# Kernel tuning notes

Hardware: AMD Instinct MI355X
Metric: run time of the kernel (lower is better)

The kernel has to match this reference:

```python
import jax, jax.numpy as jnp
import numpy as np

N_NODES = 100000


def _graph_conv(x, W, b, src, dst, deg_out, deg_in, relu):
    # DGL GraphConv, norm='both':
    #   h = (x * D_out^{-1/2}) W ; agg = scatter_sum over edges ; out = agg * D_in^{-1/2} + b
    norm_src = jax.lax.rsqrt(jnp.maximum(deg_out, 1.0))  # [N]
    norm_dst = jax.lax.rsqrt(jnp.maximum(deg_in, 1.0))   # [N]
    h = (x * norm_src[:, None]) @ W                       # [N, d_out]
    agg = jax.ops.segment_sum(h[src], dst, num_segments=N_NODES)  # [N, d_out]
    out = agg * norm_dst[:, None] + b
    return jax.nn.relu(out) if relu else out


def setup_inputs() -> dict:
    key = jax.random.key(0)
    ks = jax.random.split(key, 8)
    E = 1600000
    in_dim, hid_dim, out_dim = 128, 128, 64
    feat = jax.random.normal(ks[0], (N_NODES, in_dim), dtype=jnp.float32)
    edge_index = jax.random.randint(ks[1], (2, E), 0, N_NODES, dtype=jnp.int64)
    s = 1.0 / np.sqrt(in_dim)
    sh = 1.0 / np.sqrt(hid_dim)
    return {
        "feat": feat,
        "edge_index": edge_index,
        "W0": jax.random.normal(ks[2], (in_dim, hid_dim), dtype=jnp.float32) * s,
        "b0": jnp.zeros((hid_dim,), dtype=jnp.float32),
        "W1": jax.random.normal(ks[3], (hid_dim, hid_dim), dtype=jnp.float32) * sh,
        "b1": jnp.zeros((hid_dim,), dtype=jnp.float32),
        "W2": jax.random.normal(ks[4], (hid_dim, out_dim), dtype=jnp.float32) * sh,
        "b2": jnp.zeros((out_dim,), dtype=jnp.float32),
    }


def reference(feat, edge_index, W0, b0, W1, b1, W2, b2):
    src, dst = edge_index[0], edge_index[1]
    ones = jnp.ones(src.shape, dtype=feat.dtype)
    deg_out = jax.ops.segment_sum(ones, src, num_segments=N_NODES)  # src out-degree
    deg_in = jax.ops.segment_sum(ones, dst, num_segments=N_NODES)   # dst in-degree
    h = _graph_conv(feat, W0, b0, src, dst, deg_out, deg_in, relu=True)
    h = _graph_conv(h, W1, b1, src, dst, deg_out, deg_in, relu=True)
    h = _graph_conv(h, W2, b2, src, dst, deg_out, deg_in, relu=False)
    return h
```

## Files before the change

### kernel.cpp

```cpp
#include <hip/hip_runtime.h>
#include <hip/hip_fp16.h>


typedef _Float16 h8 __attribute__((ext_vector_type(8)));
typedef float f32x4 __attribute__((ext_vector_type(4)));

#define HWORDS 25024
#define NHS 32
#define NHD 256

__global__ __launch_bounds__(256) void k_pre(const int* __restrict__ src,
                                             const int* __restrict__ dst, int E,
                                             unsigned* __restrict__ histo_s,
                                             unsigned* __restrict__ histo_d,
                                             const float* __restrict__ W0,
                                             const float* __restrict__ W1,
                                             const float* __restrict__ W2,
                                             __half* __restrict__ Wt0,
                                             __half* __restrict__ Wt1,
                                             __half* __restrict__ Wt2) {
    __shared__ unsigned H[HWORDS];
    const int b = blockIdx.x;
    if (b < NHS + NHD) {
        const bool isS = b < NHS;
        const int c = isS ? b : b - NHS;
        const int NC = isS ? NHS : NHD;
        const int* arr = isS ? src : dst;
        unsigned* outp = (isS ? histo_s : histo_d) + (size_t)c * HWORDS;
        for (int i = threadIdx.x; i < HWORDS; i += 256) H[i] = 0;
        __syncthreads();
        const int perB = ((E + NC - 1) / NC + 3) & ~3;
        const int e0 = min(c * perB, E), e1 = min(e0 + perB, E);
        int i = e0 + threadIdx.x * 4;
        for (; i + 3 < e1; i += 1024) {
            int4 s4 = *(const int4*)(arr + i);
            atomicAdd(&H[s4.x >> 2], 1u << ((s4.x & 3) * 8));
            atomicAdd(&H[s4.y >> 2], 1u << ((s4.y & 3) * 8));
            atomicAdd(&H[s4.z >> 2], 1u << ((s4.z & 3) * 8));
            atomicAdd(&H[s4.w >> 2], 1u << ((s4.w & 3) * 8));
        }
        for (; i < e1; ++i) {
            int s = arr[i];
            atomicAdd(&H[s >> 2], 1u << ((s & 3) * 8));
        }
        __syncthreads();
        for (int i2 = threadIdx.x; i2 < HWORDS; i2 += 256) outp[i2] = H[i2];
    } else {
        int j0 = (b - NHS - NHD) * 20480;
        for (int j = j0 + threadIdx.x; j < j0 + 20480; j += 256) {
            if (j < 16384) {
                int nn = j >> 7, k = j & 127;
                Wt0[j] = __float2half(W0[k * 128 + nn]);
            } else if (j < 32768) {
                int i2 = j - 16384;
                int nn = i2 >> 7, k = i2 & 127;
                Wt1[i2] = __float2half(W1[k * 128 + nn]);
            } else if (j < 40960) {
                int i2 = j - 32768;
                int nn = i2 >> 7, k = i2 & 127;
                Wt2[i2] = __float2half(W2[k * 64 + nn]);
            }
        }
    }
}

__global__ __launch_bounds__(256) void k_scan1(const unsigned* __restrict__ histo_s,
                                               unsigned* __restrict__ histo_d,
                                               int* __restrict__ rp,
                                               int* __restrict__ bsum,
                                               float* __restrict__ ns,
                                               float* __restrict__ nd, int n) {
    __shared__ unsigned di4[64];
    __shared__ unsigned do4[64];
    const int tid = threadIdx.x, lane = tid & 63, wid = tid >> 6;
    if (tid < 64) {
        const int w = blockIdx.x * 64 + tid;
        unsigned run4 = 0;
#pragma unroll 8
        for (int b = 0; b < NHD; ++b) {
            unsigned c4 = histo_d[(size_t)b * HWORDS + w];
            histo_d[(size_t)b * HWORDS + w] = run4;
            run4 += c4;
        }
        di4[tid] = run4;
        unsigned s4 = 0;
#pragma unroll 8
        for (int b = 0; b < NHS; ++b) s4 += histo_s[(size_t)b * HWORDS + w];
        do4[tid] = s4;
    }
    __syncthreads();
    int i = blockIdx.x * 256 + tid;
    int v = 0;
    if (i < n) {
        int sh = (tid & 3) * 8;
        v = (di4[tid >> 2] >> sh) & 255;
        int dgo = (do4[tid >> 2] >> sh) & 255;
        nd[i] = rsqrtf((float)max(v, 1));
        ns[i] = rsqrtf((float)max(dgo, 1));
    }
    int x = v;
#pragma unroll
    for (int off = 1; off < 64; off <<= 1) {
        int t = __shfl_up(x, off, 64);
        if (lane >= off) x += t;
    }
    __shared__ int ws[4];
    if (lane == 63) ws[wid] = x;
    __syncthreads();
    int wo = 0;
    for (int k = 0; k < wid; ++k) wo += ws[k];
    int incl = wo + x;
    if (i < n) rp[i] = incl - v;
    if (tid == 255) bsum[blockIdx.x] = incl;
}

__global__ __launch_bounds__(512) void k_scan2(int* __restrict__ bsum, int nb,
                                               int* __restrict__ rpN) {
    __shared__ int s[512];
    const int tid = threadIdx.x;
    int v = (tid < nb) ? bsum[tid] : 0;
    s[tid] = v;
    __syncthreads();
    for (int off = 1; off < 512; off <<= 1) {
        int t = (tid >= off) ? s[tid - off] : 0;
        __syncthreads();
        s[tid] += t;
        __syncthreads();
    }
    if (tid < nb) bsum[tid] = s[tid] - v;
    if (tid == nb - 1) *rpN = v;
}

__global__ __launch_bounds__(256) void k_scatter2(const int* __restrict__ src,
                                                  const int* __restrict__ dst, int E,
                                                  const int* __restrict__ rp,
                                                  const int* __restrict__ bsum,
                                                  const unsigned* __restrict__ pfx_all,
                                                  int* __restrict__ csr) {
    __shared__ unsigned Hd[HWORDS];
    for (int i = threadIdx.x; i < HWORDS; i += 256) Hd[i] = 0;
    __syncthreads();
    const int c = blockIdx.x;
    const int perB = ((E + NHD - 1) / NHD + 3) & ~3;
    const int e0 = min(c * perB, E), e1 = min(e0 + perB, E);
    const unsigned* pfx = pfx_all + (size_t)c * HWORDS;
    int i = e0 + threadIdx.x * 4;
    for (; i + 3 < e1; i += 1024) {
        int4 d4 = *(const int4*)(dst + i);
        int4 s4 = *(const int4*)(src + i);
#define PROC(dd, ss)                                                            \
        {                                                                       \
            int sh = ((dd) & 3) * 8;                                            \
            int base = rp[dd] + bsum[(dd) >> 8] +                               \
                       (int)((pfx[(dd) >> 2] >> sh) & 255u);                    \
            unsigned old = atomicAdd(&Hd[(dd) >> 2], 1u << sh);                 \
            csr[base + (int)((old >> sh) & 255u)] = (ss);                       \
        }
        PROC(d4.x, s4.x) PROC(d4.y, s4.y) PROC(d4.z, s4.z) PROC(d4.w, s4.w)
    }
    for (; i < e1; ++i) PROC(dst[i], src[i])
#undef PROC
}

template <int BN, bool F32A>
__device__ __forceinline__ void gemm_body(const void* __restrict__ Ap,
                                          const __half* __restrict__ Wt,
                                          __half* __restrict__ C, int n, int gb) {
    constexpr int K = 128, BM = 128, LDR = K + 8;
    __shared__ __half Al[BM * LDR];
    __shared__ __half Bl[BN * LDR];
    const int tid = threadIdx.x;
    const int row0 = gb * BM;
    if (F32A) {
        const float* A = (const float*)Ap;
#pragma unroll
        for (int q = 0; q < 16; ++q) {
            int fi = q * 256 + tid;
            int r = fi >> 5, c = (fi & 31) * 4;
            int gr = row0 + r;
            float4 v = make_float4(0.f, 0.f, 0.f, 0.f);
            if (gr < n) v = *(const float4*)(A + (size_t)gr * K + c);
            __half2 h0 = __floats2half2_rn(v.x, v.y);
            __half2 h1 = __floats2half2_rn(v.z, v.w);
            uint2 pk = make_uint2(*(unsigned*)&h0, *(unsigned*)&h1);
            *(uint2*)&Al[r * LDR + c] = pk;
        }
    } else {
        const __half* A = (const __half*)Ap;
#pragma unroll
        for (int q = 0; q < 8; ++q) {
            int fi = q * 256 + tid;
            int r = fi >> 4, c = (fi & 15) * 8;
            int gr = row0 + r;
            float4 v = make_float4(0.f, 0.f, 0.f, 0.f);
            if (gr < n) v = *(const float4*)(A + (size_t)gr * K + c);
            *(float4*)&Al[r * LDR + c] = v;
        }
    }
#pragma unroll
    for (int q = 0; q < BN / 16; ++q) {
        int fi = q * 256 + tid;
        int r = fi >> 4, c = (fi & 15) * 8;
        *(float4*)&Bl[r * LDR + c] = *(const float4*)(Wt + (size_t)r * K + c);
    }
    __syncthreads();
    const int wid = tid >> 6, lane = tid & 63;
    const int lo = lane & 15, hi = lane >> 4;
    constexpr int NC = BN / 16;
    f32x4 acc[2][NC];
#pragma unroll
    for (int t = 0; t < 2; ++t)
#pragma unroll
        for (int c = 0; c < NC; ++c) acc[t][c] = (f32x4){0.f, 0.f, 0.f, 0.f};
#pragma unroll
    for (int kc = 0; kc < 4; ++kc) {
        h8 aF[2];
#pragma unroll
        for (int t = 0; t < 2; ++t)
            aF[t] = *(const h8*)&Al[(32 * wid + 16 * t + lo) * LDR + 32 * kc + 8 * hi];
#pragma unroll
        for (int c = 0; c < NC; ++c) {
            h8 bF = *(const h8*)&Bl[(16 * c + lo) * LDR + 32 * kc + 8 * hi];
#pragma unroll
            for (int t = 0; t < 2; ++t)
                acc[t][c] = __builtin_amdgcn_mfma_f32_16x16x32_f16(aF[t], bF, acc[t][c], 0, 0, 0);
        }
    }
#pragma unroll
    for (int t = 0; t < 2; ++t) {
#pragma unroll
        for (int j = 0; j < 4; ++j) {
            int gr = row0 + 32 * wid + 16 * t + 4 * hi + j;
            if (gr < n) {
#pragma unroll
                for (int c = 0; c < NC; ++c)
                    C[(size_t)gr * BN + 16 * c + lo] = __float2half(acc[t][c][j]);
            }
        }
    }
}

template <int BN, bool F32A>
__global__ __launch_bounds__(256) void k_gemm(const void* __restrict__ A,
                                              const __half* __restrict__ Wt,
                                              __half* __restrict__ C, int n) {
    gemm_body<BN, F32A>(A, Wt, C, n, blockIdx.x);
}

template <bool RELU, bool SSCALE>
__global__ __launch_bounds__(256) void k_agg128h(const __half2* __restrict__ H,
                                                 const int* __restrict__ rp,
                                                 const int* __restrict__ bsum,
                                                 const int* __restrict__ cs,
                                                 const float* __restrict__ nd,
                                                 const float* __restrict__ ns,
                                                 const float* __restrict__ b,
                                                 __half2* __restrict__ out, int n) {
    const int wid = threadIdx.x >> 6, lane = threadIdx.x & 63;
    const int node = blockIdx.x * 4 + wid;
    if (node >= n) return;
    const int beg = rp[node] + bsum[node >> 8];
    const int end = rp[node + 1] + bsum[(node + 1) >> 8];
    float2 a0 = make_float2(0.f, 0.f), a1 = a0, a2 = a0, a3 = a0;
    float2 a4 = a0, a5 = a0, a6 = a0, a7 = a0;
    for (int e = beg; e < end; e += 8) {
        int s[8];
        float w[8];
#pragma unroll
        for (int j = 0; j < 8; ++j) {
            int idx = e + j;
            int r = (idx < end) ? idx : beg;
            r = __builtin_amdgcn_readfirstlane(r);
            s[j] = cs[r];
            w[j] = (idx < end) ? 1.f : 0.f;
        }
        if (SSCALE) {
#pragma unroll
            for (int j = 0; j < 8; ++j) w[j] *= ns[s[j]];
        }
        float2 v0 = __half22float2(H[(size_t)s[0] * 64 + lane]);
        float2 v1 = __half22float2(H[(size_t)s[1] * 64 + lane]);
        float2 v2 = __half22float2(H[(size_t)s[2] * 64 + lane]);
        float2 v3 = __half22float2(H[(size_t)s[3] * 64 + lane]);
        float2 v4 = __half22float2(H[(size_t)s[4] * 64 + lane]);
        float2 v5 = __half22float2(H[(size_t)s[5] * 64 + lane]);
        float2 v6 = __half22float2(H[(size_t)s[6] * 64 + lane]);
        float2 v7 = __half22float2(H[(size_t)s[7] * 64 + lane]);
        a0.x = fmaf(v0.x, w[0], a0.x); a0.y = fmaf(v0.y, w[0], a0.y);
        a1.x = fmaf(v1.x, w[1], a1.x); a1.y = fmaf(v1.y, w[1], a1.y);
        a2.x = fmaf(v2.x, w[2], a2.x); a2.y = fmaf(v2.y, w[2], a2.y);
        a3.x = fmaf(v3.x, w[3], a3.x); a3.y = fmaf(v3.y, w[3], a3.y);
        a4.x = fmaf(v4.x, w[4], a4.x); a4.y = fmaf(v4.y, w[4], a4.y);
        a5.x = fmaf(v5.x, w[5], a5.x); a5.y = fmaf(v5.y, w[5], a5.y);
        a6.x = fmaf(v6.x, w[6], a6.x); a6.y = fmaf(v6.y, w[6], a6.y);
        a7.x = fmaf(v7.x, w[7], a7.x); a7.y = fmaf(v7.y, w[7], a7.y);
    }
    const float sc = nd[node];
    const float sn = ns[node];
    float2 bb = ((const float2*)b)[lane];
    float ax = ((a0.x + a1.x) + (a2.x + a3.x)) + ((a4.x + a5.x) + (a6.x + a7.x));
    float ay = ((a0.y + a1.y) + (a2.y + a3.y)) + ((a4.y + a5.y) + (a6.y + a7.y));
    float ox = ax * sc + bb.x;
    float oy = ay * sc + bb.y;
    if (RELU) { ox = fmaxf(ox, 0.f); oy = fmaxf(oy, 0.f); }
    ox *= sn; oy *= sn;
    out[(size_t)node * 64 + lane] = __floats2half2_rn(ox, oy);
}

__global__ __launch_bounds__(256) void k_agg64h(const __half* __restrict__ H,
                                                const int* __restrict__ rp,
                                                const int* __restrict__ bsum,
                                                const int* __restrict__ cs,
                                                const float* __restrict__ nd,
                                                const float* __restrict__ b,
                                                float* __restrict__ out, int n) {
    const int wid = threadIdx.x >> 6, lane = threadIdx.x & 63;
    const int node = blockIdx.x * 4 + wid;
    if (node >= n) return;
    const int beg = rp[node] + bsum[node >> 8];
    const int end = rp[node + 1] + bsum[(node + 1) >> 8];
    float a0 = 0.f, a1 = 0.f, a2 = 0.f, a3 = 0.f;
    float a4 = 0.f, a5 = 0.f, a6 = 0.f, a7 = 0.f;
    for (int e = beg; e < end; e += 8) {
        int s[8];
        float w[8];
#pragma unroll
        for (int j = 0; j < 8; ++j) {
            int idx = e + j;
            int r = (idx < end) ? idx : beg;
            r = __builtin_amdgcn_readfirstlane(r);
            s[j] = cs[r];
            w[j] = (idx < end) ? 1.f : 0.f;
        }
        a0 = fmaf(__half2float(H[(size_t)s[0] * 64 + lane]), w[0], a0);
        a1 = fmaf(__half2float(H[(size_t)s[1] * 64 + lane]), w[1], a1);
        a2 = fmaf(__half2float(H[(size_t)s[2] * 64 + lane]), w[2], a2);
        a3 = fmaf(__half2float(H[(size_t)s[3] * 64 + lane]), w[3], a3);
        a4 = fmaf(__half2float(H[(size_t)s[4] * 64 + lane]), w[4], a4);
        a5 = fmaf(__half2float(H[(size_t)s[5] * 64 + lane]), w[5], a5);
        a6 = fmaf(__half2float(H[(size_t)s[6] * 64 + lane]), w[6], a6);
        a7 = fmaf(__half2float(H[(size_t)s[7] * 64 + lane]), w[7], a7);
    }
    float a = ((a0 + a1) + (a2 + a3)) + ((a4 + a5) + (a6 + a7));
    out[(size_t)node * 64 + lane] = a * nd[node] + b[lane];
}

extern "C" void kernel_launch(void* const* d_in, const int* in_sizes, int n_in,
                              void* d_out, int out_size, void* d_ws, size_t ws_size,
                              hipStream_t stream) {
    const float* feat = (const float*)d_in[0];
    const int* ei = (const int*)d_in[1];
    const float* W0 = (const float*)d_in[2];
    const float* b0 = (const float*)d_in[3];
    const float* W1 = (const float*)d_in[4];
    const float* b1 = (const float*)d_in[5];
    const float* W2 = (const float*)d_in[6];
    const float* b2 = (const float*)d_in[7];
    float* out = (float*)d_out;

    const int N = in_sizes[0] / 128;
    const int E = in_sizes[1] / 2;
    const int* src = ei;
    const int* dst = ei + E;
    const int NB = (N + 255) / 256;

    char* w = (char*)d_ws;
    float* norm_src = (float*)w; w += (size_t)N * 4;
    float* norm_dst = (float*)w; w += (size_t)N * 4;
    unsigned* histo_s = (unsigned*)w; w += (size_t)NHS * HWORDS * 4;
    unsigned* histo_d = (unsigned*)w; w += (size_t)NHD * HWORDS * 4;
    int* rp    = (int*)w;        w += ((size_t)(N + 1) * 4 + 15) / 16 * 16;
    int* bsum  = (int*)w;        w += 512 * 4;
    int* csr   = (int*)w;        w += (size_t)E * 4;
    __half* Wt0 = (__half*)w;    w += 128 * 128 * 2;
    __half* Wt1 = (__half*)w;    w += 128 * 128 * 2;
    __half* Wt2 = (__half*)w;    w += 128 * 64 * 2;
    __half* Hb = (__half*)w;     w += (size_t)N * 128 * 2;
    __half* Xb = (__half*)w;     w += (size_t)N * 128 * 2;

    const int GB = (N + 127) / 128;
    const int agg_grid = (N + 3) / 4;

    k_pre<<<NHS + NHD + 2, 256, 0, stream>>>(src, dst, E, histo_s, histo_d,
                                             W0, W1, W2, Wt0, Wt1, Wt2);
    k_scan1<<<NB, 256, 0, stream>>>(histo_s, histo_d, rp, bsum, norm_src, norm_dst, N);
    k_scan2<<<1, 512, 0, stream>>>(bsum, NB, rp + N);
    k_scatter2<<<NHD, 256, 0, stream>>>(src, dst, E, rp, bsum, histo_d, csr);

    k_gemm<128, true><<<GB, 256, 0, stream>>>(feat, Wt0, Hb, N);
    k_agg128h<true, true><<<agg_grid, 256, 0, stream>>>((const __half2*)Hb, rp, bsum, csr,
                                                        norm_dst, norm_src, b0, (__half2*)Xb, N);
    k_gemm<128, false><<<GB, 256, 0, stream>>>(Xb, Wt1, Hb, N);
    k_agg128h<true, false><<<agg_grid, 256, 0, stream>>>((const __half2*)Hb, rp, bsum, csr,
                                                         norm_dst, norm_src, b1, (__half2*)Xb, N);
    k_gemm<64, false><<<GB, 256, 0, stream>>>(Xb, Wt2, Hb, N);
    k_agg64h<<<agg_grid, 256, 0, stream>>>(Hb, rp, bsum, csr, norm_dst, b2, out, N);
}
```

Measured before the change: 353.6 us.

## Partition features into 16-column slices for cache-local gather aggregation

Stores GEMM outputs and aggregation inputs in a column-sliced layout, where each 16-half slice of all nodes is contiguous, and runs aggregation per slice, with blocks interleaved across slices. Each slice's gather working set becomes small enough to stay resident in cache. The layer-0 source normalization moves into the GEMM epilogue instead of a per-edge gather multiply. Each wave now processes 16 edges at once in 8 edge slots and reduces them with shuffles. The trade-off is more blocks and more redundant CSR index reads (one pass per slice), plus narrower 4-byte gathers.

```diff
diff --git a/kernel.cpp b/kernel.cpp
--- a/kernel.cpp
+++ b/kernel.cpp
@@ -162,10 +162,11 @@
 #undef PROC
 }
 
-template <int BN, bool F32A>
+template <int BN, bool F32A, bool NSROW>
 __device__ __forceinline__ void gemm_body(const void* __restrict__ Ap,
                                           const __half* __restrict__ Wt,
-                                          __half* __restrict__ C, int n, int gb) {
+                                          const float* __restrict__ nsr,
+                                          __half* __restrict__ Cs, int n, int gb) {
     constexpr int K = 128, BM = 128, LDR = K + 8;
     __shared__ __half Al[BM * LDR];
     __shared__ __half Bl[BN * LDR];
@@ -189,12 +190,13 @@
         const __half* A = (const __half*)Ap;
 #pragma unroll
         for (int q = 0; q < 8; ++q) {
-            int fi = q * 256 + tid;
-            int r = fi >> 4, c = (fi & 15) * 8;
+            int idx = q * 256 + tid;
+            int slice = idx >> 8, rr = idx & 255;
+            int r = rr >> 1, off = (rr & 1) * 8;
             int gr = row0 + r;
             float4 v = make_float4(0.f, 0.f, 0.f, 0.f);
-            if (gr < n) v = *(const float4*)(A + (size_t)gr * K + c);
-            *(float4*)&Al[r * LDR + c] = v;
+            if (gr < n) v = *(const float4*)(A + ((size_t)slice * n + gr) * 16 + off);
+            *(float4*)&Al[r * LDR + slice * 16 + off] = v;
         }
     }
 #pragma unroll
@@ -232,82 +234,69 @@
         for (int j = 0; j < 4; ++j) {
             int gr = row0 + 32 * wid + 16 * t + 4 * hi + j;
             if (gr < n) {
+                float s = NSROW ? nsr[gr] : 1.f;
 #pragma unroll
                 for (int c = 0; c < NC; ++c)
-                    C[(size_t)gr * BN + 16 * c + lo] = __float2half(acc[t][c][j]);
+                    Cs[((size_t)c * n + gr) * 16 + lo] = __float2half(acc[t][c][j] * s);
             }
         }
     }
 }
 
-template <int BN, bool F32A>
+template <int BN, bool F32A, bool NSROW>
 __global__ __launch_bounds__(256) void k_gemm(const void* __restrict__ A,
                                               const __half* __restrict__ Wt,
-                                              __half* __restrict__ C, int n) {
-    gemm_body<BN, F32A>(A, Wt, C, n, blockIdx.x);
-}
-
-template <bool RELU, bool SSCALE>
-__global__ __launch_bounds__(256) void k_agg128h(const __half2* __restrict__ H,
+                                              const float* __restrict__ nsr,
+                                              __half* __restrict__ Cs, int n) {
+    gemm_body<BN, F32A, NSROW>(A, Wt, nsr, Cs, n, blockIdx.x);
+}
+
+__global__ __launch_bounds__(256) void k_agg128p(const __half* __restrict__ Hs,
                                                  const int* __restrict__ rp,
                                                  const int* __restrict__ bsum,
                                                  const int* __restrict__ cs,
                                                  const float* __restrict__ nd,
                                                  const float* __restrict__ ns,
                                                  const float* __restrict__ b,
-                                                 __half2* __restrict__ out, int n) {
+                                                 __half* __restrict__ Xs, int n) {
     const int wid = threadIdx.x >> 6, lane = threadIdx.x & 63;
-    const int node = blockIdx.x * 4 + wid;
+    const int p = blockIdx.x & 7;
+    const int node = (blockIdx.x >> 3) * 4 + wid;
     if (node >= n) return;
+    const int slot = lane >> 3, sub = lane & 7;
     const int beg = rp[node] + bsum[node >> 8];
     const int end = rp[node + 1] + bsum[(node + 1) >> 8];
-    float2 a0 = make_float2(0.f, 0.f), a1 = a0, a2 = a0, a3 = a0;
-    float2 a4 = a0, a5 = a0, a6 = a0, a7 = a0;
-    for (int e = beg; e < end; e += 8) {
-        int s[8];
-        float w[8];
-#pragma unroll
-        for (int j = 0; j < 8; ++j) {
-            int idx = e + j;
-            int r = (idx < end) ? idx : beg;
-            r = __builtin_amdgcn_readfirstlane(r);
-            s[j] = cs[r];
-            w[j] = (idx < end) ? 1.f : 0.f;
-        }
-        if (SSCALE) {
-#pragma unroll
-            for (int j = 0; j < 8; ++j) w[j] *= ns[s[j]];
-        }
-        float2 v0 = __half22float2(H[(size_t)s[0] * 64 + lane]);
-        float2 v1 = __half22float2(H[(size_t)s[1] * 64 + lane]);
-        float2 v2 = __half22float2(H[(size_t)s[2] * 64 + lane]);
-        float2 v3 = __half22float2(H[(size_t)s[3] * 64 + lane]);
-        float2 v4 = __half22float2(H[(size_t)s[4] * 64 + lane]);
-        float2 v5 = __half22float2(H[(size_t)s[5] * 64 + lane]);
-        float2 v6 = __half22float2(H[(size_t)s[6] * 64 + lane]);
-        float2 v7 = __half22float2(H[(size_t)s[7] * 64 + lane]);
-        a0.x = fmaf(v0.x, w[0], a0.x); a0.y = fmaf(v0.y, w[0], a0.y);
-        a1.x = fmaf(v1.x, w[1], a1.x); a1.y = fmaf(v1.y, w[1], a1.y);
-        a2.x = fmaf(v2.x, w[2], a2.x); a2.y = fmaf(v2.y, w[2], a2.y);
-        a3.x = fmaf(v3.x, w[3], a3.x); a3.y = fmaf(v3.y, w[3], a3.y);
-        a4.x = fmaf(v4.x, w[4], a4.x); a4.y = fmaf(v4.y, w[4], a4.y);
-        a5.x = fmaf(v5.x, w[5], a5.x); a5.y = fmaf(v5.y, w[5], a5.y);
-        a6.x = fmaf(v6.x, w[6], a6.x); a6.y = fmaf(v6.y, w[6], a6.y);
-        a7.x = fmaf(v7.x, w[7], a7.x); a7.y = fmaf(v7.y, w[7], a7.y);
-    }
-    const float sc = nd[node];
-    const float sn = ns[node];
-    float2 bb = ((const float2*)b)[lane];
-    float ax = ((a0.x + a1.x) + (a2.x + a3.x)) + ((a4.x + a5.x) + (a6.x + a7.x));
-    float ay = ((a0.y + a1.y) + (a2.y + a3.y)) + ((a4.y + a5.y) + (a6.y + a7.y));
-    float ox = ax * sc + bb.x;
-    float oy = ay * sc + bb.y;
-    if (RELU) { ox = fmaxf(ox, 0.f); oy = fmaxf(oy, 0.f); }
-    ox *= sn; oy *= sn;
-    out[(size_t)node * 64 + lane] = __floats2half2_rn(ox, oy);
-}
-
-__global__ __launch_bounds__(256) void k_agg64h(const __half* __restrict__ H,
+    const __half* Hp = Hs + (size_t)p * n * 16;
+    float2 a0 = make_float2(0.f, 0.f), a1 = a0;
+    for (int e = beg; e < end; e += 16) {
+        int i0 = e + slot, i1 = e + 8 + slot;
+        int r0 = (i0 < end) ? i0 : beg;
+        int r1 = (i1 < end) ? i1 : beg;
+        float w0 = (i0 < end) ? 1.f : 0.f;
+        float w1 = (i1 < end) ? 1.f : 0.f;
+        int s0 = cs[r0], s1 = cs[r1];
+        float f0 = *(const float*)(Hp + (size_t)s0 * 16 + sub * 2);
+        float f1 = *(const float*)(Hp + (size_t)s1 * 16 + sub * 2);
+        float2 v0 = __half22float2(*(__half2*)&f0);
+        float2 v1 = __half22float2(*(__half2*)&f1);
+        a0.x = fmaf(v0.x, w0, a0.x); a0.y = fmaf(v0.y, w0, a0.y);
+        a1.x = fmaf(v1.x, w1, a1.x); a1.y = fmaf(v1.y, w1, a1.y);
+    }
+    float ax = a0.x + a1.x, ay = a0.y + a1.y;
+    ax += __shfl_xor(ax, 8, 64);  ay += __shfl_xor(ay, 8, 64);
+    ax += __shfl_xor(ax, 16, 64); ay += __shfl_xor(ay, 16, 64);
+    ax += __shfl_xor(ax, 32, 64); ay += __shfl_xor(ay, 32, 64);
+    if (slot == 0) {
+        const float sc = nd[node], sn = ns[node];
+        const int col = p * 16 + sub * 2;
+        float ox = fmaxf(ax * sc + b[col], 0.f) * sn;
+        float oy = fmaxf(ay * sc + b[col + 1], 0.f) * sn;
+        __half2 h = __floats2half2_rn(ox, oy);
+        *(__half2*)(Xs + ((size_t)p * n + node) * 16 + sub * 2) = h;
+    }
+}
+
+__global__ __launch_bounds__(256) void k_agg64p(const __half* __restrict__ Hs,
                                                 const int* __restrict__ rp,
                                                 const int* __restrict__ bsum,
                                                 const int* __restrict__ cs,
@@ -315,34 +304,38 @@
                                                 const float* __restrict__ b,
                                                 float* __restrict__ out, int n) {
     const int wid = threadIdx.x >> 6, lane = threadIdx.x & 63;
-    const int node = blockIdx.x * 4 + wid;
+    const int p = blockIdx.x & 3;
+    const int node = (blockIdx.x >> 2) * 4 + wid;
     if (node >= n) return;
+    const int slot = lane >> 3, sub = lane & 7;
     const int beg = rp[node] + bsum[node >> 8];
     const int end = rp[node + 1] + bsum[(node + 1) >> 8];
-    float a0 = 0.f, a1 = 0.f, a2 = 0.f, a3 = 0.f;
-    float a4 = 0.f, a5 = 0.f, a6 = 0.f, a7 = 0.f;
-    for (int e = beg; e < end; e += 8) {
-        int s[8];
-        float w[8];
-#pragma unroll
-        for (int j = 0; j < 8; ++j) {
-            int idx = e + j;
-            int r = (idx < end) ? idx : beg;
-            r = __builtin_amdgcn_readfirstlane(r);
-            s[j] = cs[r];
-            w[j] = (idx < end) ? 1.f : 0.f;
-        }
-        a0 = fmaf(__half2float(H[(size_t)s[0] * 64 + lane]), w[0], a0);
-        a1 = fmaf(__half2float(H[(size_t)s[1] * 64 + lane]), w[1], a1);
-        a2 = fmaf(__half2float(H[(size_t)s[2] * 64 + lane]), w[2], a2);
-        a3 = fmaf(__half2float(H[(size_t)s[3] * 64 + lane]), w[3], a3);
-        a4 = fmaf(__half2float(H[(size_t)s[4] * 64 + lane]), w[4], a4);
-        a5 = fmaf(__half2float(H[(size_t)s[5] * 64 + lane]), w[5], a5);
-        a6 = fmaf(__half2float(H[(size_t)s[6] * 64 + lane]), w[6], a6);
-        a7 = fmaf(__half2float(H[(size_t)s[7] * 64 + lane]), w[7], a7);
-    }
-    float a = ((a0 + a1) + (a2 + a3)) + ((a4 + a5) + (a6 + a7));
-    out[(size_t)node * 64 + lane] = a * nd[node] + b[lane];
+    const __half* Hp = Hs + (size_t)p * n * 16;
+    float2 a0 = make_float2(0.f, 0.f), a1 = a0;
+    for (int e = beg; e < end; e += 16) {
+        int i0 = e + slot, i1 = e + 8 + slot;
+        int r0 = (i0 < end) ? i0 : beg;
+        int r1 = (i1 < end) ? i1 : beg;
+        float w0 = (i0 < end) ? 1.f : 0.f;
+        float w1 = (i1 < end) ? 1.f : 0.f;
+        int s0 = cs[r0], s1 = cs[r1];
+        float f0 = *(const float*)(Hp + (size_t)s0 * 16 + sub * 2);
+        float f1 = *(const float*)(Hp + (size_t)s1 * 16 + sub * 2);
+        float2 v0 = __half22float2(*(__half2*)&f0);
+        float2 v1 = __half22float2(*(__half2*)&f1);
+        a0.x = fmaf(v0.x, w0, a0.x); a0.y = fmaf(v0.y, w0, a0.y);
+        a1.x = fmaf(v1.x, w1, a1.x); a1.y = fmaf(v1.y, w1, a1.y);
+    }
+    float ax = a0.x + a1.x, ay = a0.y + a1.y;
+    ax += __shfl_xor(ax, 8, 64);  ay += __shfl_xor(ay, 8, 64);
+    ax += __shfl_xor(ax, 16, 64); ay += __shfl_xor(ay, 16, 64);
+    ax += __shfl_xor(ax, 32, 64); ay += __shfl_xor(ay, 32, 64);
+    if (slot == 0) {
+        const float sc = nd[node];
+        const int col = p * 16 + sub * 2;
+        float2 o = make_float2(ax * sc + b[col], ay * sc + b[col + 1]);
+        *(float2*)(out + (size_t)node * 64 + col) = o;
+    }
 }
 
 extern "C" void kernel_launch(void* const* d_in, const int* in_sizes, int n_in,
@@ -379,7 +372,7 @@
     __half* Xb = (__half*)w;     w += (size_t)N * 128 * 2;
 
     const int GB = (N + 127) / 128;
-    const int agg_grid = (N + 3) / 4;
+    const int nb4 = (N + 3) / 4;
 
     k_pre<<<NHS + NHD + 2, 256, 0, stream>>>(src, dst, E, histo_s, histo_d,
                                              W0, W1, W2, Wt0, Wt1, Wt2);
@@ -387,12 +380,10 @@
     k_scan2<<<1, 512, 0, stream>>>(bsum, NB, rp + N);
     k_scatter2<<<NHD, 256, 0, stream>>>(src, dst, E, rp, bsum, histo_d, csr);
 
-    k_gemm<128, true><<<GB, 256, 0, stream>>>(feat, Wt0, Hb, N);
-    k_agg128h<true, true><<<agg_grid, 256, 0, stream>>>((const __half2*)Hb, rp, bsum, csr,
-                                                        norm_dst, norm_src, b0, (__half2*)Xb, N);
-    k_gemm<128, false><<<GB, 256, 0, stream>>>(Xb, Wt1, Hb, N);
-    k_agg128h<true, false><<<agg_grid, 256, 0, stream>>>((const __half2*)Hb, rp, bsum, csr,
-                                                         norm_dst, norm_src, b1, (__half2*)Xb, N);
-    k_gemm<64, false><<<GB, 256, 0, stream>>>(Xb, Wt2, Hb, N);
-    k_agg64h<<<agg_grid, 256, 0, stream>>>(Hb, rp, bsum, csr, norm_dst, b2, out, N);
-}
+    k_gemm<128, true, true><<<GB, 256, 0, stream>>>(feat, Wt0, norm_src, Hb, N);
+    k_agg128p<<<nb4 * 8, 256, 0, stream>>>(Hb, rp, bsum, csr, norm_dst, norm_src, b0, Xb, N);
+    k_gemm<128, false, false><<<GB, 256, 0, stream>>>(Xb, Wt1, nullptr, Hb, N);
+    k_agg128p<<<nb4 * 8, 256, 0, stream>>>(Hb, rp, bsum, csr, norm_dst, norm_src, b1, Xb, N);
+    k_gemm<64, false, false><<<GB, 256, 0, stream>>>(Xb, Wt2, nullptr, Hb, N);
+    k_agg64p<<<nb4 * 4, 256, 0, stream>>>(Hb, rp, bsum, csr, norm_dst, b2, out, N);
+}
```

New measurement: 659.0 us. 86.4% more time.

## Fuse first-layer GEMM into preprocessing kernel and parallelize histogram scan

Applied to the files above, without the earlier changes.

The first GEMM (feat × W0) now runs inside the preprocessing kernel as extra blocks that transpose W0 into shared memory themselves. This removes one launch and lets the GEMM overlap with the degree-histogram blocks. The scan1 kernel now splits the per-word reduction over the 256 destination histograms across all four waves instead of one, which adds a shared-memory combine step. Shared memory in k_pre is sized for the histogram (about 100KB), so the GEMM blocks may run at lower occupancy.

```diff
diff --git a/kernel.cpp b/kernel.cpp
--- a/kernel.cpp
+++ b/kernel.cpp
@@ -9,21 +9,116 @@
 #define NHS 32
 #define NHD 256
 
-__global__ __launch_bounds__(256) void k_pre(const int* __restrict__ src,
-                                             const int* __restrict__ dst, int E,
-                                             unsigned* __restrict__ histo_s,
-                                             unsigned* __restrict__ histo_d,
-                                             const float* __restrict__ W0,
-                                             const float* __restrict__ W1,
-                                             const float* __restrict__ W2,
-                                             __half* __restrict__ Wt0,
-                                             __half* __restrict__ Wt1,
-                                             __half* __restrict__ Wt2) {
-    __shared__ unsigned H[HWORDS];
+template <int BN, bool F32A, bool TRANSW>
+__device__ __forceinline__ void gemm_body(const void* __restrict__ Ap,
+                                          const void* __restrict__ Wp,
+                                          __half* Al, __half* Bl,
+                                          __half* __restrict__ C, int n, int gb) {
+    constexpr int K = 128, BM = 128, LDR = K + 8;
+    const int tid = threadIdx.x;
+    const int row0 = gb * BM;
+    if (F32A) {
+        const float* A = (const float*)Ap;
+#pragma unroll
+        for (int q = 0; q < 16; ++q) {
+            int fi = q * 256 + tid;
+            int r = fi >> 5, c = (fi & 31) * 4;
+            int gr = row0 + r;
+            float4 v = make_float4(0.f, 0.f, 0.f, 0.f);
+            if (gr < n) v = *(const float4*)(A + (size_t)gr * K + c);
+            __half2 h0 = __floats2half2_rn(v.x, v.y);
+            __half2 h1 = __floats2half2_rn(v.z, v.w);
+            uint2 pk = make_uint2(*(unsigned*)&h0, *(unsigned*)&h1);
+            *(uint2*)&Al[r * LDR + c] = pk;
+        }
+    } else {
+        const __half* A = (const __half*)Ap;
+#pragma unroll
+        for (int q = 0; q < 8; ++q) {
+            int fi = q * 256 + tid;
+            int r = fi >> 4, c = (fi & 15) * 8;
+            int gr = row0 + r;
+            float4 v = make_float4(0.f, 0.f, 0.f, 0.f);
+            if (gr < n) v = *(const float4*)(A + (size_t)gr * K + c);
+            *(float4*)&Al[r * LDR + c] = v;
+        }
+    }
+    if (TRANSW) {
+        const float* W = (const float*)Wp;
+#pragma unroll
+        for (int q = 0; q < (K * BN / 4) / 256; ++q) {
+            int fi = q * 256 + tid;
+            int k = fi / (BN / 4), n4 = (fi % (BN / 4)) * 4;
+            float4 v = *(const float4*)(W + (size_t)k * BN + n4);
+            Bl[(n4 + 0) * LDR + k] = __float2half(v.x);
+            Bl[(n4 + 1) * LDR + k] = __float2half(v.y);
+            Bl[(n4 + 2) * LDR + k] = __float2half(v.z);
+            Bl[(n4 + 3) * LDR + k] = __float2half(v.w);
+        }
+    } else {
+        const __half* Wt = (const __half*)Wp;
+#pragma unroll
+        for (int q = 0; q < BN / 16; ++q) {
+            int fi = q * 256 + tid;
+            int r = fi >> 4, c = (fi & 15) * 8;
+            *(float4*)&Bl[r * LDR + c] = *(const float4*)(Wt + (size_t)r * K + c);
+        }
+    }
+    __syncthreads();
+    const int wid = tid >> 6, lane = tid & 63;
+    const int lo = lane & 15, hi = lane >> 4;
+    constexpr int NC = BN / 16;
+    f32x4 acc[2][NC];
+#pragma unroll
+    for (int t = 0; t < 2; ++t)
+#pragma unroll
+        for (int c = 0; c < NC; ++c) acc[t][c] = (f32x4){0.f, 0.f, 0.f, 0.f};
+#pragma unroll
+    for (int kc = 0; kc < 4; ++kc) {
+        h8 aF[2];
+#pragma unroll
+        for (int t = 0; t < 2; ++t)
+            aF[t] = *(const h8*)&Al[(32 * wid + 16 * t + lo) * LDR + 32 * kc + 8 * hi];
+#pragma unroll
+        for (int c = 0; c < NC; ++c) {
+            h8 bF = *(const h8*)&Bl[(16 * c + lo) * LDR + 32 * kc + 8 * hi];
+#pragma unroll
+            for (int t = 0; t < 2; ++t)
+                acc[t][c] = __builtin_amdgcn_mfma_f32_16x16x32_f16(aF[t], bF, acc[t][c], 0, 0, 0);
+        }
+    }
+#pragma unroll
+    for (int t = 0; t < 2; ++t) {
+#pragma unroll
+        for (int j = 0; j < 4; ++j) {
+            int gr = row0 + 32 * wid + 16 * t + 4 * hi + j;
+            if (gr < n) {
+#pragma unroll
+                for (int c = 0; c < NC; ++c)
+                    C[(size_t)gr * BN + 16 * c + lo] = __float2half(acc[t][c][j]);
+            }
+        }
+    }
+}
+
+__global__ __launch_bounds__(256) void k_pre(
+        const float* __restrict__ feat, const float* __restrict__ W0,
+        __half* __restrict__ Hb, int n, int GB,
+        const int* __restrict__ src, const int* __restrict__ dst, int E,
+        unsigned* __restrict__ histo_s, unsigned* __restrict__ histo_d,
+        const float* __restrict__ W1, const float* __restrict__ W2,
+        __half* __restrict__ Wt1, __half* __restrict__ Wt2) {
+    __shared__ __align__(16) char smem[HWORDS * 4];
     const int b = blockIdx.x;
-    if (b < NHS + NHD) {
-        const bool isS = b < NHS;
-        const int c = isS ? b : b - NHS;
+    if (b < GB) {
+        __half* Al = (__half*)smem;
+        __half* Bl = (__half*)(smem + 128 * 136 * 2);
+        gemm_body<128, true, true>(feat, W0, Al, Bl, Hb, n, b);
+    } else if (b < GB + NHS + NHD) {
+        unsigned* H = (unsigned*)smem;
+        const int hb = b - GB;
+        const bool isS = hb < NHS;
+        const int c = isS ? hb : hb - NHS;
         const int NC = isS ? NHS : NHD;
         const int* arr = isS ? src : dst;
         unsigned* outp = (isS ? histo_s : histo_d) + (size_t)c * HWORDS;
@@ -46,17 +141,13 @@
         __syncthreads();
         for (int i2 = threadIdx.x; i2 < HWORDS; i2 += 256) outp[i2] = H[i2];
     } else {
-        int j0 = (b - NHS - NHD) * 20480;
-        for (int j = j0 + threadIdx.x; j < j0 + 20480; j += 256) {
+        int j0 = (b - GB - NHS - NHD) * 12288;
+        for (int j = j0 + threadIdx.x; j < j0 + 12288; j += 256) {
             if (j < 16384) {
                 int nn = j >> 7, k = j & 127;
-                Wt0[j] = __float2half(W0[k * 128 + nn]);
-            } else if (j < 32768) {
+                Wt1[j] = __float2half(W1[k * 128 + nn]);
+            } else if (j < 24576) {
                 int i2 = j - 16384;
-                int nn = i2 >> 7, k = i2 & 127;
-                Wt1[i2] = __float2half(W1[k * 128 + nn]);
-            } else if (j < 40960) {
-                int i2 = j - 32768;
                 int nn = i2 >> 7, k = i2 & 127;
                 Wt2[i2] = __float2half(W2[k * 64 + nn]);
             }
@@ -70,23 +161,38 @@
                                                int* __restrict__ bsum,
                                                float* __restrict__ ns,
                                                float* __restrict__ nd, int n) {
+    __shared__ unsigned qsd[4][64];
+    __shared__ unsigned qss[4][64];
     __shared__ unsigned di4[64];
     __shared__ unsigned do4[64];
-    const int tid = threadIdx.x, lane = tid & 63, wid = tid >> 6;
-    if (tid < 64) {
-        const int w = blockIdx.x * 64 + tid;
-        unsigned run4 = 0;
+    const int tid = threadIdx.x, lane = tid & 63, q = tid >> 6;
+    const int w = blockIdx.x * 64 + lane;
+    {
+        unsigned s = 0;
 #pragma unroll 8
-        for (int b = 0; b < NHD; ++b) {
+        for (int b = q * 64; b < (q + 1) * 64; ++b)
+            s += histo_d[(size_t)b * HWORDS + w];
+        qsd[q][lane] = s;
+        unsigned s2 = 0;
+#pragma unroll
+        for (int b = q * 8; b < (q + 1) * 8; ++b)
+            s2 += histo_s[(size_t)b * HWORDS + w];
+        qss[q][lane] = s2;
+    }
+    __syncthreads();
+    if (q == 0) {
+        di4[lane] = qsd[0][lane] + qsd[1][lane] + qsd[2][lane] + qsd[3][lane];
+        do4[lane] = qss[0][lane] + qss[1][lane] + qss[2][lane] + qss[3][lane];
+    }
+    {
+        unsigned run = 0;
+        for (int k = 0; k < q; ++k) run += qsd[k][lane];
+#pragma unroll 8
+        for (int b = q * 64; b < (q + 1) * 64; ++b) {
             unsigned c4 = histo_d[(size_t)b * HWORDS + w];
-            histo_d[(size_t)b * HWORDS + w] = run4;
-            run4 += c4;
-        }
-        di4[tid] = run4;
-        unsigned s4 = 0;
-#pragma unroll 8
-        for (int b = 0; b < NHS; ++b) s4 += histo_s[(size_t)b * HWORDS + w];
-        do4[tid] = s4;
+            histo_d[(size_t)b * HWORDS + w] = run;
+            run += c4;
+        }
     }
     __syncthreads();
     int i = blockIdx.x * 256 + tid;
@@ -105,10 +211,10 @@
         if (lane >= off) x += t;
     }
     __shared__ int ws[4];
-    if (lane == 63) ws[wid] = x;
+    if (lane == 63) ws[q] = x;
     __syncthreads();
     int wo = 0;
-    for (int k = 0; k < wid; ++k) wo += ws[k];
+    for (int k = 0; k < q; ++k) wo += ws[k];
     int incl = wo + x;
     if (i < n) rp[i] = incl - v;
     if (tid == 255) bsum[blockIdx.x] = incl;
@@ -163,88 +269,12 @@
 }
 
 template <int BN, bool F32A>
-__device__ __forceinline__ void gemm_body(const void* __restrict__ Ap,
-                                          const __half* __restrict__ Wt,
-                                          __half* __restrict__ C, int n, int gb) {
-    constexpr int K = 128, BM = 128, LDR = K + 8;
-    __shared__ __half Al[BM * LDR];
-    __shared__ __half Bl[BN * LDR];
-    const int tid = threadIdx.x;
-    const int row0 = gb * BM;
-    if (F32A) {
-        const float* A = (const float*)Ap;
-#pragma unroll
-        for (int q = 0; q < 16; ++q) {
-            int fi = q * 256 + tid;
-            int r = fi >> 5, c = (fi & 31) * 4;
-            int gr = row0 + r;
-            float4 v = make_float4(0.f, 0.f, 0.f, 0.f);
-            if (gr < n) v = *(const float4*)(A + (size_t)gr * K + c);
-            __half2 h0 = __floats2half2_rn(v.x, v.y);
-            __half2 h1 = __floats2half2_rn(v.z, v.w);
-            uint2 pk = make_uint2(*(unsigned*)&h0, *(unsigned*)&h1);
-            *(uint2*)&Al[r * LDR + c] = pk;
-        }
-    } else {
-        const __half* A = (const __half*)Ap;
-#pragma unroll
-        for (int q = 0; q < 8; ++q) {
-            int fi = q * 256 + tid;
-            int r = fi >> 4, c = (fi & 15) * 8;
-            int gr = row0 + r;
-            float4 v = make_float4(0.f, 0.f, 0.f, 0.f);
-            if (gr < n) v = *(const float4*)(A + (size_t)gr * K + c);
-            *(float4*)&Al[r * LDR + c] = v;
-        }
-    }
-#pragma unroll
-    for (int q = 0; q < BN / 16; ++q) {
-        int fi = q * 256 + tid;
-        int r = fi >> 4, c = (fi & 15) * 8;
-        *(float4*)&Bl[r * LDR + c] = *(const float4*)(Wt + (size_t)r * K + c);
-    }
-    __syncthreads();
-    const int wid = tid >> 6, lane = tid & 63;
-    const int lo = lane & 15, hi = lane >> 4;
-    constexpr int NC = BN / 16;
-    f32x4 acc[2][NC];
-#pragma unroll
-    for (int t = 0; t < 2; ++t)
-#pragma unroll
-        for (int c = 0; c < NC; ++c) acc[t][c] = (f32x4){0.f, 0.f, 0.f, 0.f};
-#pragma unroll
-    for (int kc = 0; kc < 4; ++kc) {
-        h8 aF[2];
-#pragma unroll
-        for (int t = 0; t < 2; ++t)
-            aF[t] = *(const h8*)&Al[(32 * wid + 16 * t + lo) * LDR + 32 * kc + 8 * hi];
-#pragma unroll
-        for (int c = 0; c < NC; ++c) {
-            h8 bF = *(const h8*)&Bl[(16 * c + lo) * LDR + 32 * kc + 8 * hi];
-#pragma unroll
-            for (int t = 0; t < 2; ++t)
-                acc[t][c] = __builtin_amdgcn_mfma_f32_16x16x32_f16(aF[t], bF, acc[t][c], 0, 0, 0);
-        }
-    }
-#pragma unroll
-    for (int t = 0; t < 2; ++t) {
-#pragma unroll
-        for (int j = 0; j < 4; ++j) {
-            int gr = row0 + 32 * wid + 16 * t + 4 * hi + j;
-            if (gr < n) {
-#pragma unroll
-                for (int c = 0; c < NC; ++c)
-                    C[(size_t)gr * BN + 16 * c + lo] = __float2half(acc[t][c][j]);
-            }
-        }
-    }
-}
-
-template <int BN, bool F32A>
 __global__ __launch_bounds__(256) void k_gemm(const void* __restrict__ A,
                                               const __half* __restrict__ Wt,
                                               __half* __restrict__ C, int n) {
-    gemm_body<BN, F32A>(A, Wt, C, n, blockIdx.x);
+    __shared__ __half Al[128 * 136];
+    __shared__ __half Bl[BN * 136];
+    gemm_body<BN, F32A, false>(A, Wt, Al, Bl, C, n, blockIdx.x);
 }
 
 template <bool RELU, bool SSCALE>
@@ -372,7 +402,6 @@
     int* rp    = (int*)w;        w += ((size_t)(N + 1) * 4 + 15) / 16 * 16;
     int* bsum  = (int*)w;        w += 512 * 4;
     int* csr   = (int*)w;        w += (size_t)E * 4;
-    __half* Wt0 = (__half*)w;    w += 128 * 128 * 2;
     __half* Wt1 = (__half*)w;    w += 128 * 128 * 2;
     __half* Wt2 = (__half*)w;    w += 128 * 64 * 2;
     __half* Hb = (__half*)w;     w += (size_t)N * 128 * 2;
@@ -381,13 +410,13 @@
     const int GB = (N + 127) / 128;
     const int agg_grid = (N + 3) / 4;
 
-    k_pre<<<NHS + NHD + 2, 256, 0, stream>>>(src, dst, E, histo_s, histo_d,
-                                             W0, W1, W2, Wt0, Wt1, Wt2);
+    k_pre<<<GB + NHS + NHD + 2, 256, 0, stream>>>(feat, W0, Hb, N, GB,
+                                                  src, dst, E, histo_s, histo_d,
+                                                  W1, W2, Wt1, Wt2);
     k_scan1<<<NB, 256, 0, stream>>>(histo_s, histo_d, rp, bsum, norm_src, norm_dst, N);
     k_scan2<<<1, 512, 0, stream>>>(bsum, NB, rp + N);
     k_scatter2<<<NHD, 256, 0, stream>>>(src, dst, E, rp, bsum, histo_d, csr);
 
-    k_gemm<128, true><<<GB, 256, 0, stream>>>(feat, Wt0, Hb, N);
     k_agg128h<true, true><<<agg_grid, 256, 0, stream>>>((const __half2*)Hb, rp, bsum, csr,
                                                         norm_dst, norm_src, b0, (__half2*)Xb, N);
     k_gemm<128, false><<<GB, 256, 0, stream>>>(Xb, Wt1, Hb, N);
```

Measured after the change: 357.5 us. No clear change (+1.1%).

## Widen histogram/scatter blocks to 1024 threads and parallelize scan1 column prefix

Applied to the files above, without the earlier changes.

Histogram and CSR scatter kernels now use 1024-thread blocks, so each shared-memory histogram is filled by more waves, and the source histogram gets twice as many chunks. The first scan kernel splits the 256-chunk column prefix across all four waves instead of one. This reads histo_d twice, once to sum and once to write prefixes. The intent is to cut the latency of the serial preprocessing stages, at the cost of more shared-atomic contention per block and the extra pass over histo_d.

```diff
diff --git a/kernel.cpp b/kernel.cpp
--- a/kernel.cpp
+++ b/kernel.cpp
@@ -6,33 +6,34 @@
 typedef float f32x4 __attribute__((ext_vector_type(4)));
 
 #define HWORDS 25024
-#define NHS 32
+#define NHS 64
 #define NHD 256
 
-__global__ __launch_bounds__(256) void k_pre(const int* __restrict__ src,
-                                             const int* __restrict__ dst, int E,
-                                             unsigned* __restrict__ histo_s,
-                                             unsigned* __restrict__ histo_d,
-                                             const float* __restrict__ W0,
-                                             const float* __restrict__ W1,
-                                             const float* __restrict__ W2,
-                                             __half* __restrict__ Wt0,
-                                             __half* __restrict__ Wt1,
-                                             __half* __restrict__ Wt2) {
+__global__ __launch_bounds__(1024) void k_pre(const int* __restrict__ src,
+                                              const int* __restrict__ dst, int E,
+                                              unsigned* __restrict__ histo_s,
+                                              unsigned* __restrict__ histo_d,
+                                              const float* __restrict__ W0,
+                                              const float* __restrict__ W1,
+                                              const float* __restrict__ W2,
+                                              __half* __restrict__ Wt0,
+                                              __half* __restrict__ Wt1,
+                                              __half* __restrict__ Wt2) {
     __shared__ unsigned H[HWORDS];
     const int b = blockIdx.x;
+    const int tid = threadIdx.x;
     if (b < NHS + NHD) {
         const bool isS = b < NHS;
         const int c = isS ? b : b - NHS;
         const int NC = isS ? NHS : NHD;
         const int* arr = isS ? src : dst;
         unsigned* outp = (isS ? histo_s : histo_d) + (size_t)c * HWORDS;
-        for (int i = threadIdx.x; i < HWORDS; i += 256) H[i] = 0;
+        for (int i = tid; i < HWORDS; i += 1024) H[i] = 0;
         __syncthreads();
         const int perB = ((E + NC - 1) / NC + 3) & ~3;
         const int e0 = min(c * perB, E), e1 = min(e0 + perB, E);
-        int i = e0 + threadIdx.x * 4;
-        for (; i + 3 < e1; i += 1024) {
+        int i = e0 + tid * 4;
+        for (; i + 3 < e1; i += 4096) {
             int4 s4 = *(const int4*)(arr + i);
             atomicAdd(&H[s4.x >> 2], 1u << ((s4.x & 3) * 8));
             atomicAdd(&H[s4.y >> 2], 1u << ((s4.y & 3) * 8));
@@ -44,10 +45,9 @@
             atomicAdd(&H[s >> 2], 1u << ((s & 3) * 8));
         }
         __syncthreads();
-        for (int i2 = threadIdx.x; i2 < HWORDS; i2 += 256) outp[i2] = H[i2];
+        for (int i2 = tid; i2 < HWORDS; i2 += 1024) outp[i2] = H[i2];
     } else {
-        int j0 = (b - NHS - NHD) * 20480;
-        for (int j = j0 + threadIdx.x; j < j0 + 20480; j += 256) {
+        for (int j = tid; j < 40960; j += 1024) {
             if (j < 16384) {
                 int nn = j >> 7, k = j & 127;
                 Wt0[j] = __float2half(W0[k * 128 + nn]);
@@ -55,7 +55,7 @@
                 int i2 = j - 16384;
                 int nn = i2 >> 7, k = i2 & 127;
                 Wt1[i2] = __float2half(W1[k * 128 + nn]);
-            } else if (j < 40960) {
+            } else {
                 int i2 = j - 32768;
                 int nn = i2 >> 7, k = i2 & 127;
                 Wt2[i2] = __float2half(W2[k * 64 + nn]);
@@ -70,23 +70,38 @@
                                                int* __restrict__ bsum,
                                                float* __restrict__ ns,
                                                float* __restrict__ nd, int n) {
+    __shared__ unsigned qsd[4][64];
+    __shared__ unsigned qss[4][64];
     __shared__ unsigned di4[64];
     __shared__ unsigned do4[64];
-    const int tid = threadIdx.x, lane = tid & 63, wid = tid >> 6;
-    if (tid < 64) {
-        const int w = blockIdx.x * 64 + tid;
-        unsigned run4 = 0;
+    const int tid = threadIdx.x, lane = tid & 63, q = tid >> 6;
+    const int w = blockIdx.x * 64 + lane;
+    {
+        unsigned s = 0;
 #pragma unroll 8
-        for (int b = 0; b < NHD; ++b) {
+        for (int b = q * (NHD / 4); b < (q + 1) * (NHD / 4); ++b)
+            s += histo_d[(size_t)b * HWORDS + w];
+        qsd[q][lane] = s;
+        unsigned s2 = 0;
+#pragma unroll
+        for (int b = q * (NHS / 4); b < (q + 1) * (NHS / 4); ++b)
+            s2 += histo_s[(size_t)b * HWORDS + w];
+        qss[q][lane] = s2;
+    }
+    __syncthreads();
+    if (q == 0) {
+        di4[lane] = qsd[0][lane] + qsd[1][lane] + qsd[2][lane] + qsd[3][lane];
+        do4[lane] = qss[0][lane] + qss[1][lane] + qss[2][lane] + qss[3][lane];
+    }
+    {
+        unsigned run = 0;
+        for (int k = 0; k < q; ++k) run += qsd[k][lane];
+#pragma unroll 8
+        for (int b = q * (NHD / 4); b < (q + 1) * (NHD / 4); ++b) {
             unsigned c4 = histo_d[(size_t)b * HWORDS + w];
-            histo_d[(size_t)b * HWORDS + w] = run4;
-            run4 += c4;
-        }
-        di4[tid] = run4;
-        unsigned s4 = 0;
-#pragma unroll 8
-        for (int b = 0; b < NHS; ++b) s4 += histo_s[(size_t)b * HWORDS + w];
-        do4[tid] = s4;
+            histo_d[(size_t)b * HWORDS + w] = run;
+            run += c4;
+        }
     }
     __syncthreads();
     int i = blockIdx.x * 256 + tid;
@@ -105,10 +120,10 @@
         if (lane >= off) x += t;
     }
     __shared__ int ws[4];
-    if (lane == 63) ws[wid] = x;
+    if (lane == 63) ws[q] = x;
     __syncthreads();
     int wo = 0;
-    for (int k = 0; k < wid; ++k) wo += ws[k];
+    for (int k = 0; k < q; ++k) wo += ws[k];
     int incl = wo + x;
     if (i < n) rp[i] = incl - v;
     if (tid == 255) bsum[blockIdx.x] = incl;
@@ -131,21 +146,22 @@
     if (tid == nb - 1) *rpN = v;
 }
 
-__global__ __launch_bounds__(256) void k_scatter2(const int* __restrict__ src,
-                                                  const int* __restrict__ dst, int E,
-                                                  const int* __restrict__ rp,
-                                                  const int* __restrict__ bsum,
-                                                  const unsigned* __restrict__ pfx_all,
-                                                  int* __restrict__ csr) {
+__global__ __launch_bounds__(1024) void k_scatter2(const int* __restrict__ src,
+                                                   const int* __restrict__ dst, int E,
+                                                   const int* __restrict__ rp,
+                                                   const int* __restrict__ bsum,
+                                                   const unsigned* __restrict__ pfx_all,
+                                                   int* __restrict__ csr) {
     __shared__ unsigned Hd[HWORDS];
-    for (int i = threadIdx.x; i < HWORDS; i += 256) Hd[i] = 0;
+    const int tid = threadIdx.x;
+    for (int i = tid; i < HWORDS; i += 1024) Hd[i] = 0;
     __syncthreads();
     const int c = blockIdx.x;
     const int perB = ((E + NHD - 1) / NHD + 3) & ~3;
     const int e0 = min(c * perB, E), e1 = min(e0 + perB, E);
     const unsigned* pfx = pfx_all + (size_t)c * HWORDS;
-    int i = e0 + threadIdx.x * 4;
-    for (; i + 3 < e1; i += 1024) {
+    int i = e0 + tid * 4;
+    for (; i + 3 < e1; i += 4096) {
         int4 d4 = *(const int4*)(dst + i);
         int4 s4 = *(const int4*)(src + i);
 #define PROC(dd, ss)                                                            \
@@ -381,11 +397,11 @@
     const int GB = (N + 127) / 128;
     const int agg_grid = (N + 3) / 4;
 
-    k_pre<<<NHS + NHD + 2, 256, 0, stream>>>(src, dst, E, histo_s, histo_d,
-                                             W0, W1, W2, Wt0, Wt1, Wt2);
+    k_pre<<<NHS + NHD + 1, 1024, 0, stream>>>(src, dst, E, histo_s, histo_d,
+                                              W0, W1, W2, Wt0, Wt1, Wt2);
     k_scan1<<<NB, 256, 0, stream>>>(histo_s, histo_d, rp, bsum, norm_src, norm_dst, N);
     k_scan2<<<1, 512, 0, stream>>>(bsum, NB, rp + N);
-    k_scatter2<<<NHD, 256, 0, stream>>>(src, dst, E, rp, bsum, histo_d, csr);
+    k_scatter2<<<NHD, 1024, 0, stream>>>(src, dst, E, rp, bsum, histo_d, csr);
 
     k_gemm<128, true><<<GB, 256, 0, stream>>>(feat, Wt0, Hb, N);
     k_agg128h<true, true><<<agg_grid, 256, 0, stream>>>((const __half2*)Hb, rp, bsum, csr,
```

Result: no change. 348.8 us (-1.3%).
